# Performance work log

Measured on AMD Instinct MI355X. Metric: run time of the kernel, lower is better.

Reference implementation:

```python
import jax, jax.numpy as jnp
import numpy as np
import math

F, M, C, OUT = 60, 600, 8, 18  # feature_size, max_samples, cluster_size, output_dim
B = 2048


def l2_normalize(x, axis):
    # matches tf.nn.l2_normalize (epsilon=1e-12)
    sq = jnp.sum(jnp.square(x), axis=axis, keepdims=True)
    return x * jax.lax.rsqrt(jnp.maximum(sq, 1e-12))


def setup_inputs() -> dict:
    key = jax.random.key(0)
    k = jax.random.split(key, 6)
    s1 = 1.0 / math.sqrt(F)
    s2 = 1.0 / math.sqrt(C)
    return {
        "reshaped_input": jax.random.normal(k[0], (B * M, F), dtype=jnp.float32),
        "cluster_weights": jax.random.normal(k[1], (F, C), dtype=jnp.float32) * s1,
        "covar_weights": jax.random.normal(k[2], (F, C), dtype=jnp.float32) * s1,
        "cluster_biases": jax.random.normal(k[3], (C,), dtype=jnp.float32) * s1,
        "cluster_weights2": jax.random.normal(k[4], (1, F, C), dtype=jnp.float32) * s1,
        "hidden1_weights": jax.random.normal(k[5], (2 * C * F, OUT), dtype=jnp.float32) * s2,
    }


def reference(reshaped_input, cluster_weights, covar_weights, cluster_biases,
              cluster_weights2, hidden1_weights):
    cw = jnp.square(covar_weights) + 1e-6                      # [F, C]

    act = reshaped_input @ cluster_weights + cluster_biases    # [B*M, C]
    act = jax.nn.softmax(act, axis=-1)
    act = act.reshape(-1, M, C)                                # [B, M, C]

    a_sum = jnp.sum(act, axis=-2, keepdims=True)               # [B, 1, C]
    a = a_sum * cluster_weights2                               # [B, F, C]

    x = reshaped_input.reshape(-1, M, F)                       # [B, M, F]

    fv1 = jnp.einsum('bmc,bmf->bfc', act, x)                   # [B, F, C]
    fv2 = jnp.einsum('bmc,bmf->bfc', act, jnp.square(x))       # [B, F, C]

    a2 = a_sum * jnp.square(cluster_weights2)                  # [B, F, C]
    b2 = fv1 * cluster_weights2                                # [B, F, C]

    fv2 = a2 + fv2 - 2.0 * b2
    fv2 = fv2 / jnp.square(cw)
    fv2 = fv2 - a_sum                                          # broadcast [B,1,C]
    fv2 = fv2.reshape(-1, C * F)
    fv2 = l2_normalize(fv2, axis=1)
    fv2 = l2_normalize(fv2, axis=1)  # second normalize as in original (idempotent)

    fv1 = (fv1 - a) / cw                                       # [B, F, C]
    fv1 = l2_normalize(fv1, axis=1)                            # per-cluster, along F
    fv1 = fv1.reshape(-1, C * F)
    fv1 = l2_normalize(fv1, axis=1)

    fv = jnp.concatenate([fv1, fv2], axis=1)                   # [B, 2*C*F]
    return fv @ hidden1_weights                                # [B, OUT]
```

## Files before the change

### kernel.cpp

```cpp
#include <hip/hip_runtime.h>
#include <hip/hip_bf16.h>

#define FDIM 60
#define MROW 600
#define CDIM 8
#define ODIM 18
#define CH   120
#define NCHUNK 5
#define BLK  512

typedef short bf16x8 __attribute__((ext_vector_type(8)));
typedef float f32x4  __attribute__((ext_vector_type(4)));

__device__ __forceinline__ unsigned int pk2(float lo, float hi) {
    __hip_bfloat162 h2 = __float22bfloat162_rn(make_float2(lo, hi));
    unsigned int u;
    __builtin_memcpy(&u, &h2, sizeof(u));
    return u;
}
__device__ __forceinline__ short f2bf(float f) {
    __hip_bfloat16 h = __float2bfloat16(f);
    short s;
    __builtin_memcpy(&s, &h, sizeof(s));
    return s;
}

#define WAVE_LGKM() do {                                          \
    asm volatile("s_waitcnt lgkmcnt(0)" ::: "memory");            \
    __builtin_amdgcn_sched_barrier(0);                            \
} while (0)
#define RAW_BAR() do {                                            \
    asm volatile("s_waitcnt lgkmcnt(0)" ::: "memory");            \
    __builtin_amdgcn_s_barrier();                                 \
    __builtin_amdgcn_sched_barrier(0);                            \
} while (0)

__global__ void __launch_bounds__(BLK, 6) netfv_kernel(
    const float* __restrict__ x,
    const float* __restrict__ W,
    const float* __restrict__ covar,
    const float* __restrict__ bias,
    const float* __restrict__ cw2,
    const float* __restrict__ H,
    float* __restrict__ out)
{
    __shared__ __align__(16) short xsT1[64 * 136];
    __shared__ __align__(16) short xsM [120 * 72];
    __shared__ __align__(16) short actT[16 * 136];
    __shared__ __align__(16) short WtB [16 * 72];

    float* const fvbuf = (float*)xsT1;
    float* const fvl   = (float*)xsT1 + 1024;
    float* const redA  = (float*)actT;
    float* const redB  = redA + 64;
    float* const asuml = redB + 64;
    float* const n1rs  = asuml + 8;
    float* const n1c_s = n1rs + 8;
    float* const n2c_s = n1c_s + 8;
    float* const scal  = n2c_s + 8;

    const int tid  = threadIdx.x;
    const int b    = blockIdx.x;
    const int lane = tid & 63;
    const int wv   = tid >> 6;
    const int mg   = tid >> 3;
    const int fs   = tid & 7;
    const int ln15 = lane & 15;
    const int quad = lane >> 4;
    const int fvsel = wv & 1;
    const int tile  = wv >> 1;

    const size_t rowbase = (size_t)b * (MROW * FDIM);
    const bool stv = (mg < 60);
    const float* prow = x + rowbase + (size_t)(2 * mg) * FDIM + 8 * fs;
    const int mloc = wv * 16 + ln15;
    const bool vm = (mloc < CH);
    const int mrow = vm ? mloc : 0;

    float4 A0, A1, B0, B1;
    A0 = A1 = B0 = B1 = make_float4(0.f, 0.f, 0.f, 0.f);
    if (stv) {
        A0 = *(const float4*)prow;
        A1 = *(const float4*)(prow + FDIM);
        if (fs < 7) { B0 = *(const float4*)(prow + 4); B1 = *(const float4*)(prow + FDIM + 4); }
    }

    {
        int c = tid >> 5, j = tid & 31;
        float v0 = (2 * j     < FDIM) ? W[(2 * j) * CDIM + (c & 7)]     : 0.f;
        float v1 = (2 * j + 1 < FDIM) ? W[(2 * j + 1) * CDIM + (c & 7)] : 0.f;
        if (c >= CDIM) { v0 = 0.f; v1 = 0.f; }
        ((unsigned int*)WtB)[c * 36 + j] = pk2(v0, v1);
    }
    {
        unsigned int* z1 = (unsigned int*)xsT1;
        for (int i = tid; i < 64 * 68; i += BLK) z1[i] = 0u;
        unsigned int* az = (unsigned int*)(actT + 8 * 136);
        for (int i = tid; i < 544; i += BLK) az[i] = 0u;
    }
    __syncthreads();

    const bf16x8 aw0 = *(const bf16x8*)(WtB + ln15 * 72 + quad * 8);
    const bf16x8 aw1 = *(const bf16x8*)(WtB + ln15 * 72 + 32 + quad * 8);
    const float4 lb  = *(const float4*)(bias + (quad & 1) * 4);

    f32x4 acc = {0.f, 0.f, 0.f, 0.f};
    float asum_acc[4] = {0.f, 0.f, 0.f, 0.f};

    for (int ck = 0; ck < NCHUNK; ++ck) {
        if (stv) {
            float xv0[8] = {A0.x, A0.y, A0.z, A0.w, B0.x, B0.y, B0.z, B0.w};
            float xv1[8] = {A1.x, A1.y, A1.z, A1.w, B1.x, B1.y, B1.z, B1.w};
            {
                unsigned int q0 = pk2(xv0[0], xv0[1]), q1 = pk2(xv0[2], xv0[3]);
                unsigned int q2 = pk2(xv0[4], xv0[5]), q3 = pk2(xv0[6], xv0[7]);
                *(uint4*)(xsM + (2 * mg) * 72 + 8 * fs) = make_uint4(q0, q1, q2, q3);
                unsigned int s0 = pk2(xv1[0], xv1[1]), s1 = pk2(xv1[2], xv1[3]);
                unsigned int s2 = pk2(xv1[4], xv1[5]), s3 = pk2(xv1[6], xv1[7]);
                *(uint4*)(xsM + (2 * mg + 1) * 72 + 8 * fs) = make_uint4(s0, s1, s2, s3);
            }
            const int wbase = (((mg >> 2) ^ fs) << 2) + (mg & 3);
            #pragma unroll
            for (int i = 0; i < 8; ++i) {
                int woff = (8 * fs + i) * 68 + wbase;
                ((unsigned int*)xsT1)[woff] = pk2(xv0[i], xv1[i]);
            }
        }
        __builtin_amdgcn_sched_barrier(0);

        float4 nA0, nA1, nB0, nB1;
        nA0 = nA1 = nB0 = nB1 = make_float4(0.f, 0.f, 0.f, 0.f);
        if (ck + 1 < NCHUNK && stv) {
            const float* pn = prow + (size_t)(ck + 1) * (CH * FDIM);
            nA0 = *(const float4*)pn;
            nA1 = *(const float4*)(pn + FDIM);
            if (fs < 7) { nB0 = *(const float4*)(pn + 4); nB1 = *(const float4*)(pn + FDIM + 4); }
        }

        WAVE_LGKM();
        {
            bf16x8 bv0 = *(const bf16x8*)(xsM + mrow * 72 + quad * 8);
            bf16x8 bv1 = *(const bf16x8*)(xsM + mrow * 72 + 32 + quad * 8);
            f32x4 lz = {0.f, 0.f, 0.f, 0.f};
            lz = __builtin_amdgcn_mfma_f32_16x16x32_bf16(aw0, bv0, lz, 0, 0, 0);
            lz = __builtin_amdgcn_mfma_f32_16x16x32_bf16(aw1, bv1, lz, 0, 0, 0);
            float L0 = lz[0] + lb.x, L1 = lz[1] + lb.y;
            float L2 = lz[2] + lb.z, L3 = lz[3] + lb.w;
            float mx = fmaxf(fmaxf(L0, L1), fmaxf(L2, L3));
            mx = fmaxf(mx, __shfl_xor(mx, 16));
            float e0 = __expf(L0 - mx), e1 = __expf(L1 - mx);
            float e2 = __expf(L2 - mx), e3 = __expf(L3 - mx);
            float s = e0 + e1 + e2 + e3;
            s += __shfl_xor(s, 16);
            float inv = __builtin_amdgcn_rcpf(s);
            if (quad < 2) {
                float a0  = vm ? e0 * inv : 0.f, a1v = vm ? e1 * inv : 0.f;
                float a2v = vm ? e2 * inv : 0.f, a3v = vm ? e3 * inv : 0.f;
                asum_acc[0] += a0;  asum_acc[1] += a1v;
                asum_acc[2] += a2v; asum_acc[3] += a3v;
                actT[(quad * 4 + 0) * 136 + mloc] = f2bf(a0);
                actT[(quad * 4 + 1) * 136 + mloc] = f2bf(a1v);
                actT[(quad * 4 + 2) * 136 + mloc] = f2bf(a2v);
                actT[(quad * 4 + 3) * 136 + mloc] = f2bf(a3v);
            }
        }
        RAW_BAR();

        {
            const int f   = tile * 16 + ln15;
            const int fsw = f >> 3;
            #pragma unroll
            for (int ks = 0; ks < 4; ++ks) {
                bf16x8 av = *(const bf16x8*)(actT + ln15 * 136 + ks * 32 + quad * 8);
                int kblk = ks * 4 + quad;
                bf16x8 bv = *(const bf16x8*)(xsT1 + f * 136 + ((kblk ^ fsw) << 3));
                if (fvsel) {
                    union { bf16x8 v; unsigned short us[8]; unsigned int u[4]; } in, sq;
                    in.v = bv;
                    #pragma unroll
                    for (int p = 0; p < 4; ++p) {
                        float lo = __uint_as_float((unsigned)in.us[2 * p]     << 16);
                        float hi = __uint_as_float((unsigned)in.us[2 * p + 1] << 16);
                        sq.u[p] = pk2(lo * lo, hi * hi);
                    }
                    bv = sq.v;
                }
                acc = __builtin_amdgcn_mfma_f32_16x16x32_bf16(av, bv, acc, 0, 0, 0);
            }
        }
        RAW_BAR();

        A0 = nA0; A1 = nA1; B0 = nB0; B1 = nB1;
    }

    #pragma unroll
    for (int r = 0; r < 4; ++r) {
        float v = asum_acc[r];
        v += __shfl_xor(v, 1); v += __shfl_xor(v, 2);
        v += __shfl_xor(v, 4); v += __shfl_xor(v, 8);
        asum_acc[r] = v;
    }
    if (quad < 2 && ln15 == 0) {
        #pragma unroll
        for (int r = 0; r < 4; ++r) redA[wv * 8 + quad * 4 + r] = asum_acc[r];
    }
    __syncthreads();
    if (tid < 64) {
        float v = redA[tid];
        v += __shfl_down(v, 8); v += __shfl_down(v, 16); v += __shfl_down(v, 32);
        if (tid < 8) asuml[tid] = v;
    }
    if (quad < 2) {
        #pragma unroll
        for (int r = 0; r < 4; ++r)
            fvbuf[fvsel * 512 + (tile * 16 + ln15) * 8 + quad * 4 + r] = acc[r];
    }
    __syncthreads();

    float fv1v = 0.f, fv2v = 0.f;
    const int f_e = tid >> 3, c_e = tid & 7;
    if (tid < 480) {
        float fv1r = fvbuf[f_e * 8 + c_e];
        float fv2r = fvbuf[512 + f_e * 8 + c_e];
        float asv  = asuml[c_e];
        float cw2v = cw2[f_e * 8 + c_e];
        float cv   = covar[f_e * 8 + c_e];
        float cwv  = cv * cv + 1e-6f;
        float rcw  = 1.0f / cwv;
        fv1v = (fv1r - asv * cw2v) * rcw;
        fv2v = (fmaf(asv * cw2v, cw2v, fv2r) - 2.0f * fv1r * cw2v) * rcw * rcw - asv;
    }

    {
        float p1 = fv1v * fv1v, p2 = fv2v * fv2v;
        p1 += __shfl_down(p1, 8);  p2 += __shfl_down(p2, 8);
        p1 += __shfl_down(p1, 16); p2 += __shfl_down(p2, 16);
        p1 += __shfl_down(p1, 32); p2 += __shfl_down(p2, 32);
        if (lane < 8) { redA[wv * 8 + lane] = p1; redB[wv * 8 + lane] = p2; }
    }
    __syncthreads();
    if (tid < 64) {
        float q1 = redA[tid], q2 = redB[tid];
        q1 += __shfl_down(q1, 8);  q2 += __shfl_down(q2, 8);
        q1 += __shfl_down(q1, 16); q2 += __shfl_down(q2, 16);
        q1 += __shfl_down(q1, 32); q2 += __shfl_down(q2, 32);
        if (tid < 8) { n1c_s[tid] = q1; n2c_s[tid] = q2; }
    }
    __syncthreads();
    if (tid == 0) {
        float S1 = 0.f, S2 = 0.f;
        #pragma unroll
        for (int c = 0; c < 8; ++c) {
            float rs = rsqrtf(fmaxf(n1c_s[c], 1e-12f));
            n1rs[c] = rs;
            S1 += n1c_s[c] * rs * rs;
            S2 += n2c_s[c];
        }
        scal[0] = rsqrtf(fmaxf(S1, 1e-12f));
        scal[1] = rsqrtf(fmaxf(S2, 1e-12f));
    }
    __syncthreads();
    if (tid < 480) {
        fvl[f_e * 8 + c_e]       = fv1v * n1rs[c_e] * scal[0];
        fvl[480 + f_e * 8 + c_e] = fv2v * scal[1];
    }
    __syncthreads();

    for (int o = wv; o < ODIM; o += 8) {
        float sacc = 0.f;
        #pragma unroll 5
        for (int i = lane; i < 960; i += 64)
            sacc = fmaf(fvl[i], H[i * ODIM + o], sacc);
        sacc += __shfl_down(sacc, 32);
        sacc += __shfl_down(sacc, 16);
        sacc += __shfl_down(sacc, 8);
        sacc += __shfl_down(sacc, 4);
        sacc += __shfl_down(sacc, 2);
        sacc += __shfl_down(sacc, 1);
        if (lane == 0) out[(size_t)b * ODIM + o] = sacc;
    }
}

extern "C" void kernel_launch(void* const* d_in, const int* in_sizes, int n_in,
                              void* d_out, int out_size, void* d_ws, size_t ws_size,
                              hipStream_t stream) {
    const float* x     = (const float*)d_in[0];
    const float* W     = (const float*)d_in[1];
    const float* covar = (const float*)d_in[2];
    const float* bias  = (const float*)d_in[3];
    const float* cw2   = (const float*)d_in[4];
    const float* H     = (const float*)d_in[5];
    float* outp = (float*)d_out;

    const int Bn = in_sizes[0] / (MROW * FDIM);
    hipLaunchKernelGGL(netfv_kernel, dim3(Bn), dim3(BLK), 0, stream,
                       x, W, covar, bias, cw2, H, outp);
}
```

Before: 430.9 us.

## Make kernel persistent with grid-stride over batches and cross-batch prefetch

Launches a fixed grid of 768 blocks that loop over batch items, prefetching the first chunk of the next batch during the last chunk of the current one. This removes the per-block launch and prologue cost and hides the global-load latency at batch boundaries. In exchange it adds extra barriers and must re-zero the part of shared memory that the epilogue overwrote. With 2048 batches spread over 768 blocks, the last wave of work is uneven (some blocks do 3 items, others 2).

```diff
diff --git a/kernel.cpp b/kernel.cpp
--- a/kernel.cpp
+++ b/kernel.cpp
@@ -8,6 +8,7 @@
 #define CH   120
 #define NCHUNK 5
 #define BLK  512
+#define NBLK 768
 
 typedef short bf16x8 __attribute__((ext_vector_type(8)));
 typedef float f32x4  __attribute__((ext_vector_type(4)));
@@ -42,7 +43,8 @@
     const float* __restrict__ bias,
     const float* __restrict__ cw2,
     const float* __restrict__ H,
-    float* __restrict__ out)
+    float* __restrict__ out,
+    int Bn)
 {
     __shared__ __align__(16) short xsT1[64 * 136];
     __shared__ __align__(16) short xsM [120 * 72];
@@ -60,7 +62,6 @@
     float* const scal  = n2c_s + 8;
 
     const int tid  = threadIdx.x;
-    const int b    = blockIdx.x;
     const int lane = tid & 63;
     const int wv   = tid >> 6;
     const int mg   = tid >> 3;
@@ -70,19 +71,21 @@
     const int fvsel = wv & 1;
     const int tile  = wv >> 1;
 
-    const size_t rowbase = (size_t)b * (MROW * FDIM);
     const bool stv = (mg < 60);
-    const float* prow = x + rowbase + (size_t)(2 * mg) * FDIM + 8 * fs;
+    const int xoff = 2 * mg * FDIM + 8 * fs;
     const int mloc = wv * 16 + ln15;
     const bool vm = (mloc < CH);
     const int mrow = vm ? mloc : 0;
 
+    int nb = blockIdx.x;
+
     float4 A0, A1, B0, B1;
     A0 = A1 = B0 = B1 = make_float4(0.f, 0.f, 0.f, 0.f);
-    if (stv) {
-        A0 = *(const float4*)prow;
-        A1 = *(const float4*)(prow + FDIM);
-        if (fs < 7) { B0 = *(const float4*)(prow + 4); B1 = *(const float4*)(prow + FDIM + 4); }
+    if (nb < Bn && stv) {
+        const float* p0 = x + (size_t)nb * (MROW * FDIM) + xoff;
+        A0 = *(const float4*)p0;
+        A1 = *(const float4*)(p0 + FDIM);
+        if (fs < 7) { B0 = *(const float4*)(p0 + 4); B1 = *(const float4*)(p0 + FDIM + 4); }
     }
 
     {
@@ -104,180 +107,201 @@
     const bf16x8 aw1 = *(const bf16x8*)(WtB + ln15 * 72 + 32 + quad * 8);
     const float4 lb  = *(const float4*)(bias + (quad & 1) * 4);
 
-    f32x4 acc = {0.f, 0.f, 0.f, 0.f};
-    float asum_acc[4] = {0.f, 0.f, 0.f, 0.f};
-
-    for (int ck = 0; ck < NCHUNK; ++ck) {
-        if (stv) {
-            float xv0[8] = {A0.x, A0.y, A0.z, A0.w, B0.x, B0.y, B0.z, B0.w};
-            float xv1[8] = {A1.x, A1.y, A1.z, A1.w, B1.x, B1.y, B1.z, B1.w};
+    while (nb < Bn) {
+        const int nbn = nb + NBLK;
+        const float* prow = x + (size_t)nb * (MROW * FDIM) + xoff;
+
+        f32x4 acc = {0.f, 0.f, 0.f, 0.f};
+        float asum_acc[4] = {0.f, 0.f, 0.f, 0.f};
+
+        for (int ck = 0; ck < NCHUNK; ++ck) {
+            if (stv) {
+                float xv0[8] = {A0.x, A0.y, A0.z, A0.w, B0.x, B0.y, B0.z, B0.w};
+                float xv1[8] = {A1.x, A1.y, A1.z, A1.w, B1.x, B1.y, B1.z, B1.w};
+                {
+                    unsigned int q0 = pk2(xv0[0], xv0[1]), q1 = pk2(xv0[2], xv0[3]);
+                    unsigned int q2 = pk2(xv0[4], xv0[5]), q3 = pk2(xv0[6], xv0[7]);
+                    *(uint4*)(xsM + (2 * mg) * 72 + 8 * fs) = make_uint4(q0, q1, q2, q3);
+                    unsigned int s0 = pk2(xv1[0], xv1[1]), s1 = pk2(xv1[2], xv1[3]);
+                    unsigned int s2 = pk2(xv1[4], xv1[5]), s3 = pk2(xv1[6], xv1[7]);
+                    *(uint4*)(xsM + (2 * mg + 1) * 72 + 8 * fs) = make_uint4(s0, s1, s2, s3);
+                }
+                const int wbase = (((mg >> 2) ^ fs) << 2) + (mg & 3);
+                #pragma unroll
+                for (int i = 0; i < 8; ++i) {
+                    int woff = (8 * fs + i) * 68 + wbase;
+                    ((unsigned int*)xsT1)[woff] = pk2(xv0[i], xv1[i]);
+                }
+            }
+            __builtin_amdgcn_sched_barrier(0);
+
+            float4 nA0, nA1, nB0, nB1;
+            nA0 = nA1 = nB0 = nB1 = make_float4(0.f, 0.f, 0.f, 0.f);
+            if (stv) {
+                if (ck + 1 < NCHUNK) {
+                    const float* pn = prow + (size_t)(ck + 1) * (CH * FDIM);
+                    nA0 = *(const float4*)pn;
+                    nA1 = *(const float4*)(pn + FDIM);
+                    if (fs < 7) { nB0 = *(const float4*)(pn + 4); nB1 = *(const float4*)(pn + FDIM + 4); }
+                } else if (nbn < Bn) {
+                    const float* pn = x + (size_t)nbn * (MROW * FDIM) + xoff;
+                    nA0 = *(const float4*)pn;
+                    nA1 = *(const float4*)(pn + FDIM);
+                    if (fs < 7) { nB0 = *(const float4*)(pn + 4); nB1 = *(const float4*)(pn + FDIM + 4); }
+                }
+            }
+
+            WAVE_LGKM();
             {
-                unsigned int q0 = pk2(xv0[0], xv0[1]), q1 = pk2(xv0[2], xv0[3]);
-                unsigned int q2 = pk2(xv0[4], xv0[5]), q3 = pk2(xv0[6], xv0[7]);
-                *(uint4*)(xsM + (2 * mg) * 72 + 8 * fs) = make_uint4(q0, q1, q2, q3);
-                unsigned int s0 = pk2(xv1[0], xv1[1]), s1 = pk2(xv1[2], xv1[3]);
-                unsigned int s2 = pk2(xv1[4], xv1[5]), s3 = pk2(xv1[6], xv1[7]);
-                *(uint4*)(xsM + (2 * mg + 1) * 72 + 8 * fs) = make_uint4(s0, s1, s2, s3);
-            }
-            const int wbase = (((mg >> 2) ^ fs) << 2) + (mg & 3);
+                bf16x8 bv0 = *(const bf16x8*)(xsM + mrow * 72 + quad * 8);
+                bf16x8 bv1 = *(const bf16x8*)(xsM + mrow * 72 + 32 + quad * 8);
+                f32x4 lz = {0.f, 0.f, 0.f, 0.f};
+                lz = __builtin_amdgcn_mfma_f32_16x16x32_bf16(aw0, bv0, lz, 0, 0, 0);
+                lz = __builtin_amdgcn_mfma_f32_16x16x32_bf16(aw1, bv1, lz, 0, 0, 0);
+                float L0 = lz[0] + lb.x, L1 = lz[1] + lb.y;
+                float L2 = lz[2] + lb.z, L3 = lz[3] + lb.w;
+                float mx = fmaxf(fmaxf(L0, L1), fmaxf(L2, L3));
+                mx = fmaxf(mx, __shfl_xor(mx, 16));
+                float e0 = __expf(L0 - mx), e1 = __expf(L1 - mx);
+                float e2 = __expf(L2 - mx), e3 = __expf(L3 - mx);
+                float s = e0 + e1 + e2 + e3;
+                s += __shfl_xor(s, 16);
+                float inv = __builtin_amdgcn_rcpf(s);
+                if (quad < 2) {
+                    float a0  = vm ? e0 * inv : 0.f, a1v = vm ? e1 * inv : 0.f;
+                    float a2v = vm ? e2 * inv : 0.f, a3v = vm ? e3 * inv : 0.f;
+                    asum_acc[0] += a0;  asum_acc[1] += a1v;
+                    asum_acc[2] += a2v; asum_acc[3] += a3v;
+                    actT[(quad * 4 + 0) * 136 + mloc] = f2bf(a0);
+                    actT[(quad * 4 + 1) * 136 + mloc] = f2bf(a1v);
+                    actT[(quad * 4 + 2) * 136 + mloc] = f2bf(a2v);
+                    actT[(quad * 4 + 3) * 136 + mloc] = f2bf(a3v);
+                }
+            }
+            RAW_BAR();
+
+            {
+                const int f   = tile * 16 + ln15;
+                const int fsw = f >> 3;
+                #pragma unroll
+                for (int ks = 0; ks < 4; ++ks) {
+                    bf16x8 av = *(const bf16x8*)(actT + ln15 * 136 + ks * 32 + quad * 8);
+                    int kblk = ks * 4 + quad;
+                    bf16x8 bv = *(const bf16x8*)(xsT1 + f * 136 + ((kblk ^ fsw) << 3));
+                    if (fvsel) {
+                        union { bf16x8 v; unsigned short us[8]; unsigned int u[4]; } in, sq;
+                        in.v = bv;
+                        #pragma unroll
+                        for (int p = 0; p < 4; ++p) {
+                            float lo = __uint_as_float((unsigned)in.us[2 * p]     << 16);
+                            float hi = __uint_as_float((unsigned)in.us[2 * p + 1] << 16);
+                            sq.u[p] = pk2(lo * lo, hi * hi);
+                        }
+                        bv = sq.v;
+                    }
+                    acc = __builtin_amdgcn_mfma_f32_16x16x32_bf16(av, bv, acc, 0, 0, 0);
+                }
+            }
+            RAW_BAR();
+
+            A0 = nA0; A1 = nA1; B0 = nB0; B1 = nB1;
+        }
+
+        #pragma unroll
+        for (int r = 0; r < 4; ++r) {
+            float v = asum_acc[r];
+            v += __shfl_xor(v, 1); v += __shfl_xor(v, 2);
+            v += __shfl_xor(v, 4); v += __shfl_xor(v, 8);
+            asum_acc[r] = v;
+        }
+        if (quad < 2 && ln15 == 0) {
             #pragma unroll
-            for (int i = 0; i < 8; ++i) {
-                int woff = (8 * fs + i) * 68 + wbase;
-                ((unsigned int*)xsT1)[woff] = pk2(xv0[i], xv1[i]);
-            }
-        }
-        __builtin_amdgcn_sched_barrier(0);
-
-        float4 nA0, nA1, nB0, nB1;
-        nA0 = nA1 = nB0 = nB1 = make_float4(0.f, 0.f, 0.f, 0.f);
-        if (ck + 1 < NCHUNK && stv) {
-            const float* pn = prow + (size_t)(ck + 1) * (CH * FDIM);
-            nA0 = *(const float4*)pn;
-            nA1 = *(const float4*)(pn + FDIM);
-            if (fs < 7) { nB0 = *(const float4*)(pn + 4); nB1 = *(const float4*)(pn + FDIM + 4); }
-        }
-
-        WAVE_LGKM();
+            for (int r = 0; r < 4; ++r) redA[wv * 8 + quad * 4 + r] = asum_acc[r];
+        }
+        RAW_BAR();
+        if (tid < 64) {
+            float v = redA[tid];
+            v += __shfl_down(v, 8); v += __shfl_down(v, 16); v += __shfl_down(v, 32);
+            if (tid < 8) asuml[tid] = v;
+        }
+        if (quad < 2) {
+            #pragma unroll
+            for (int r = 0; r < 4; ++r)
+                fvbuf[fvsel * 512 + (tile * 16 + ln15) * 8 + quad * 4 + r] = acc[r];
+        }
+        RAW_BAR();
+
+        float fv1v = 0.f, fv2v = 0.f;
+        const int f_e = tid >> 3, c_e = tid & 7;
+        if (tid < 480) {
+            float fv1r = fvbuf[f_e * 8 + c_e];
+            float fv2r = fvbuf[512 + f_e * 8 + c_e];
+            float asv  = asuml[c_e];
+            float cw2v = cw2[f_e * 8 + c_e];
+            float cv   = covar[f_e * 8 + c_e];
+            float cwv  = cv * cv + 1e-6f;
+            float rcw  = 1.0f / cwv;
+            fv1v = (fv1r - asv * cw2v) * rcw;
+            fv2v = (fmaf(asv * cw2v, cw2v, fv2r) - 2.0f * fv1r * cw2v) * rcw * rcw - asv;
+        }
+
         {
-            bf16x8 bv0 = *(const bf16x8*)(xsM + mrow * 72 + quad * 8);
-            bf16x8 bv1 = *(const bf16x8*)(xsM + mrow * 72 + 32 + quad * 8);
-            f32x4 lz = {0.f, 0.f, 0.f, 0.f};
-            lz = __builtin_amdgcn_mfma_f32_16x16x32_bf16(aw0, bv0, lz, 0, 0, 0);
-            lz = __builtin_amdgcn_mfma_f32_16x16x32_bf16(aw1, bv1, lz, 0, 0, 0);
-            float L0 = lz[0] + lb.x, L1 = lz[1] + lb.y;
-            float L2 = lz[2] + lb.z, L3 = lz[3] + lb.w;
-            float mx = fmaxf(fmaxf(L0, L1), fmaxf(L2, L3));
-            mx = fmaxf(mx, __shfl_xor(mx, 16));
-            float e0 = __expf(L0 - mx), e1 = __expf(L1 - mx);
-            float e2 = __expf(L2 - mx), e3 = __expf(L3 - mx);
-            float s = e0 + e1 + e2 + e3;
-            s += __shfl_xor(s, 16);
-            float inv = __builtin_amdgcn_rcpf(s);
-            if (quad < 2) {
-                float a0  = vm ? e0 * inv : 0.f, a1v = vm ? e1 * inv : 0.f;
-                float a2v = vm ? e2 * inv : 0.f, a3v = vm ? e3 * inv : 0.f;
-                asum_acc[0] += a0;  asum_acc[1] += a1v;
-                asum_acc[2] += a2v; asum_acc[3] += a3v;
-                actT[(quad * 4 + 0) * 136 + mloc] = f2bf(a0);
-                actT[(quad * 4 + 1) * 136 + mloc] = f2bf(a1v);
-                actT[(quad * 4 + 2) * 136 + mloc] = f2bf(a2v);
-                actT[(quad * 4 + 3) * 136 + mloc] = f2bf(a3v);
-            }
-        }
-        RAW_BAR();
-
+            float p1 = fv1v * fv1v, p2 = fv2v * fv2v;
+            p1 += __shfl_down(p1, 8);  p2 += __shfl_down(p2, 8);
+            p1 += __shfl_down(p1, 16); p2 += __shfl_down(p2, 16);
+            p1 += __shfl_down(p1, 32); p2 += __shfl_down(p2, 32);
+            if (lane < 8) { redA[wv * 8 + lane] = p1; redB[wv * 8 + lane] = p2; }
+        }
+        RAW_BAR();
+        if (tid < 64) {
+            float q1 = redA[tid], q2 = redB[tid];
+            q1 += __shfl_down(q1, 8);  q2 += __shfl_down(q2, 8);
+            q1 += __shfl_down(q1, 16); q2 += __shfl_down(q2, 16);
+            q1 += __shfl_down(q1, 32); q2 += __shfl_down(q2, 32);
+            if (tid < 8) { n1c_s[tid] = q1; n2c_s[tid] = q2; }
+        }
+        RAW_BAR();
+        if (tid == 0) {
+            float S1 = 0.f, S2 = 0.f;
+            #pragma unroll
+            for (int c = 0; c < 8; ++c) {
+                float rs = rsqrtf(fmaxf(n1c_s[c], 1e-12f));
+                n1rs[c] = rs;
+                S1 += n1c_s[c] * rs * rs;
+                S2 += n2c_s[c];
+            }
+            scal[0] = rsqrtf(fmaxf(S1, 1e-12f));
+            scal[1] = rsqrtf(fmaxf(S2, 1e-12f));
+        }
+        RAW_BAR();
+        if (tid < 480) {
+            fvl[f_e * 8 + c_e]       = fv1v * n1rs[c_e] * scal[0];
+            fvl[480 + f_e * 8 + c_e] = fv2v * scal[1];
+        }
+        RAW_BAR();
+
+        for (int o = wv; o < ODIM; o += 8) {
+            float sacc = 0.f;
+            #pragma unroll 5
+            for (int i = lane; i < 960; i += 64)
+                sacc = fmaf(fvl[i], H[i * ODIM + o], sacc);
+            sacc += __shfl_down(sacc, 32);
+            sacc += __shfl_down(sacc, 16);
+            sacc += __shfl_down(sacc, 8);
+            sacc += __shfl_down(sacc, 4);
+            sacc += __shfl_down(sacc, 2);
+            sacc += __shfl_down(sacc, 1);
+            if (lane == 0) out[(size_t)nb * ODIM + o] = sacc;
+        }
+
+        RAW_BAR();
         {
-            const int f   = tile * 16 + ln15;
-            const int fsw = f >> 3;
-            #pragma unroll
-            for (int ks = 0; ks < 4; ++ks) {
-                bf16x8 av = *(const bf16x8*)(actT + ln15 * 136 + ks * 32 + quad * 8);
-                int kblk = ks * 4 + quad;
-                bf16x8 bv = *(const bf16x8*)(xsT1 + f * 136 + ((kblk ^ fsw) << 3));
-                if (fvsel) {
-                    union { bf16x8 v; unsigned short us[8]; unsigned int u[4]; } in, sq;
-                    in.v = bv;
-                    #pragma unroll
-                    for (int p = 0; p < 4; ++p) {
-                        float lo = __uint_as_float((unsigned)in.us[2 * p]     << 16);
-                        float hi = __uint_as_float((unsigned)in.us[2 * p + 1] << 16);
-                        sq.u[p] = pk2(lo * lo, hi * hi);
-                    }
-                    bv = sq.v;
-                }
-                acc = __builtin_amdgcn_mfma_f32_16x16x32_bf16(av, bv, acc, 0, 0, 0);
-            }
-        }
-        RAW_BAR();
-
-        A0 = nA0; A1 = nA1; B0 = nB0; B1 = nB1;
-    }
-
-    #pragma unroll
-    for (int r = 0; r < 4; ++r) {
-        float v = asum_acc[r];
-        v += __shfl_xor(v, 1); v += __shfl_xor(v, 2);
-        v += __shfl_xor(v, 4); v += __shfl_xor(v, 8);
-        asum_acc[r] = v;
-    }
-    if (quad < 2 && ln15 == 0) {
-        #pragma unroll
-        for (int r = 0; r < 4; ++r) redA[wv * 8 + quad * 4 + r] = asum_acc[r];
-    }
-    __syncthreads();
-    if (tid < 64) {
-        float v = redA[tid];
-        v += __shfl_down(v, 8); v += __shfl_down(v, 16); v += __shfl_down(v, 32);
-        if (tid < 8) asuml[tid] = v;
-    }
-    if (quad < 2) {
-        #pragma unroll
-        for (int r = 0; r < 4; ++r)
-            fvbuf[fvsel * 512 + (tile * 16 + ln15) * 8 + quad * 4 + r] = acc[r];
-    }
-    __syncthreads();
-
-    float fv1v = 0.f, fv2v = 0.f;
-    const int f_e = tid >> 3, c_e = tid & 7;
-    if (tid < 480) {
-        float fv1r = fvbuf[f_e * 8 + c_e];
-        float fv2r = fvbuf[512 + f_e * 8 + c_e];
-        float asv  = asuml[c_e];
-        float cw2v = cw2[f_e * 8 + c_e];
-        float cv   = covar[f_e * 8 + c_e];
-        float cwv  = cv * cv + 1e-6f;
-        float rcw  = 1.0f / cwv;
-        fv1v = (fv1r - asv * cw2v) * rcw;
-        fv2v = (fmaf(asv * cw2v, cw2v, fv2r) - 2.0f * fv1r * cw2v) * rcw * rcw - asv;
-    }
-
-    {
-        float p1 = fv1v * fv1v, p2 = fv2v * fv2v;
-        p1 += __shfl_down(p1, 8);  p2 += __shfl_down(p2, 8);
-        p1 += __shfl_down(p1, 16); p2 += __shfl_down(p2, 16);
-        p1 += __shfl_down(p1, 32); p2 += __shfl_down(p2, 32);
-        if (lane < 8) { redA[wv * 8 + lane] = p1; redB[wv * 8 + lane] = p2; }
-    }
-    __syncthreads();
-    if (tid < 64) {
-        float q1 = redA[tid], q2 = redB[tid];
-        q1 += __shfl_down(q1, 8);  q2 += __shfl_down(q2, 8);
-        q1 += __shfl_down(q1, 16); q2 += __shfl_down(q2, 16);
-        q1 += __shfl_down(q1, 32); q2 += __shfl_down(q2, 32);
-        if (tid < 8) { n1c_s[tid] = q1; n2c_s[tid] = q2; }
-    }
-    __syncthreads();
-    if (tid == 0) {
-        float S1 = 0.f, S2 = 0.f;
-        #pragma unroll
-        for (int c = 0; c < 8; ++c) {
-            float rs = rsqrtf(fmaxf(n1c_s[c], 1e-12f));
-            n1rs[c] = rs;
-            S1 += n1c_s[c] * rs * rs;
-            S2 += n2c_s[c];
-        }
-        scal[0] = rsqrtf(fmaxf(S1, 1e-12f));
-        scal[1] = rsqrtf(fmaxf(S2, 1e-12f));
-    }
-    __syncthreads();
-    if (tid < 480) {
-        fvl[f_e * 8 + c_e]       = fv1v * n1rs[c_e] * scal[0];
-        fvl[480 + f_e * 8 + c_e] = fv2v * scal[1];
-    }
-    __syncthreads();
-
-    for (int o = wv; o < ODIM; o += 8) {
-        float sacc = 0.f;
-        #pragma unroll 5
-        for (int i = lane; i < 960; i += 64)
-            sacc = fmaf(fvl[i], H[i * ODIM + o], sacc);
-        sacc += __shfl_down(sacc, 32);
-        sacc += __shfl_down(sacc, 16);
-        sacc += __shfl_down(sacc, 8);
-        sacc += __shfl_down(sacc, 4);
-        sacc += __shfl_down(sacc, 2);
-        sacc += __shfl_down(sacc, 1);
-        if (lane == 0) out[(size_t)b * ODIM + o] = sacc;
+            unsigned int* z1 = (unsigned int*)xsT1;
+            for (int i = tid; i < 1984; i += BLK) z1[i] = 0u;
+        }
+        RAW_BAR();
+
+        nb = nbn;
     }
 }
 
@@ -293,6 +317,7 @@
     float* outp = (float*)d_out;
 
     const int Bn = in_sizes[0] / (MROW * FDIM);
-    hipLaunchKernelGGL(netfv_kernel, dim3(Bn), dim3(BLK), 0, stream,
-                       x, W, covar, bias, cw2, H, outp);
+    const int grid = (Bn < NBLK) ? Bn : NBLK;
+    hipLaunchKernelGGL(netfv_kernel, dim3(grid), dim3(BLK), 0, stream,
+                       x, W, covar, bias, cw2, H, outp, Bn);
 }
```

New measurement: 448.5 us. 1.04x slower.
